# Performance work log

Hardware: AMD Instinct MI355X
Metric: run time of the kernel (lower is better)

## Reference

```python
import jax, jax.numpy as jnp
import numpy as np

B, N, D, E = 4, 4096, 1024, 64
EPS = 1e-9
THRESH = 0.2            # second_threshold_eval
CAP_FACTOR = 2.0        # capacity_factor_eval
MIN_EXPERT_CAPACITY = 4


def setup_inputs() -> dict:
    key = jax.random.key(0)
    k1, k2 = jax.random.split(key)
    x = jax.random.normal(k1, (B, N, D), dtype=jnp.float32)
    w_gating = jax.random.normal(k2, (D, E), dtype=jnp.float32)
    return {"x": x, "w_gating": w_gating}


def _cumsum_exclusive(t, axis):
    # exclusive cumsum along `axis` (equivalent to pad-then-cumsum-then-slice)
    return jnp.cumsum(t, axis=axis) - t


def _gating(x, w_gating):
    b, n, d = x.shape
    e = w_gating.shape[-1]
    dt = x.dtype

    gate_logits = jnp.einsum('bnd,de->bne', x, w_gating)   # [b,n,e]
    raw_gates = jax.nn.softmax(gate_logits, axis=-1)

    index_1 = jnp.argmax(raw_gates, axis=-1)               # [b,n]
    gate_1 = jnp.max(raw_gates, axis=-1)                   # [b,n]
    mask_1 = jax.nn.one_hot(index_1, e, dtype=dt)          # [b,n,e]
    density_1_proxy = raw_gates

    gates_without_top_1 = raw_gates * (1.0 - mask_1)
    index_2 = jnp.argmax(gates_without_top_1, axis=-1)
    gate_2 = jnp.max(gates_without_top_1, axis=-1)
    mask_2 = jax.nn.one_hot(index_2, e, dtype=dt)

    denom = gate_1 + gate_2 + EPS
    gate_1 = gate_1 / denom
    gate_2 = gate_2 / denom

    # load-balancing aux loss
    density_1 = jnp.mean(mask_1, axis=-2)                  # [b,e]
    density_proxy = jnp.mean(density_1_proxy, axis=-2)     # [b,e]
    loss = jnp.mean(density_proxy * density_1) * float(e * e)

    # second-expert policy: 'threshold'
    mask_2 = mask_2 * (gate_2 > THRESH).astype(dt)[..., None]

    expert_capacity = max(min(n, int(n * CAP_FACTOR / e)), MIN_EXPERT_CAPACITY)
    cap_f = float(expert_capacity)

    # capacity routing for top-1
    position_in_expert_1 = _cumsum_exclusive(mask_1, axis=-2) * mask_1
    mask_1 = mask_1 * (position_in_expert_1 < cap_f).astype(dt)
    mask_1_count = jnp.sum(mask_1, axis=-2, keepdims=True)  # [b,1,e]
    mask_1_flat = jnp.sum(mask_1, axis=-1)                  # [b,n]
    position_in_expert_1 = jnp.sum(position_in_expert_1, axis=-1)  # [b,n]
    gate_1 = gate_1 * mask_1_flat

    # capacity routing for top-2 (offset by top-1 counts)
    position_in_expert_2 = (_cumsum_exclusive(mask_2, axis=-2) + mask_1_count) * mask_2
    mask_2 = mask_2 * (position_in_expert_2 < cap_f).astype(dt)
    mask_2_flat = jnp.sum(mask_2, axis=-1)
    position_in_expert_2 = jnp.sum(position_in_expert_2, axis=-1)
    gate_2 = gate_2 * mask_2_flat

    # one_hot with out-of-range index -> all zeros, matching safe_one_hot's clipping
    oh_e1 = jax.nn.one_hot(index_1, e, dtype=dt)
    oh_e2 = jax.nn.one_hot(index_2, e, dtype=dt)
    oh_c1 = jax.nn.one_hot(position_in_expert_1.astype(jnp.int32), expert_capacity, dtype=dt)
    oh_c2 = jax.nn.one_hot(position_in_expert_2.astype(jnp.int32), expert_capacity, dtype=dt)

    combine_tensor = (
        (gate_1 * mask_1_flat)[..., None, None] * oh_e1[..., :, None] * oh_c1[..., None, :]
        + (gate_2 * mask_2_flat)[..., None, None] * oh_e2[..., :, None] * oh_c2[..., None, :]
    )  # [b,n,e,capacity]

    router_z_loss = jnp.mean(jnp.sum(jax.nn.logsumexp(gate_logits, axis=-1), axis=-1))
    return combine_tensor, loss, router_z_loss


def reference(x, w_gating):
    combine_tensor, loss, router_z_loss = _gating(x, w_gating)
    dispatch_tensor = (combine_tensor != 0).astype(combine_tensor.dtype)
    return dispatch_tensor, combine_tensor, loss, router_z_loss
```

## Files before the change

kernel.cpp:

```cpp
#include <hip/hip_runtime.h>


#define B_DIM 4
#define N_DIM 4096
#define D_DIM 1024
#define E_DIM 64
#define CAP   128
#define NTOK  (B_DIM * N_DIM)
#define TM    32
#define TK    64

#define WS_IDX1  0
#define WS_IDX2  65536
#define WS_G1    131072
#define WS_G2    196608
#define WS_POS1  262144
#define WS_POS2  327680
#define WS_CNT1  393216
#define WS_DENS  394240
#define WS_ZSUM  395264

__global__ __launch_bounds__(256) void gating_kernel(
    const float* __restrict__ x, const float* __restrict__ w,
    int* __restrict__ idx1, int* __restrict__ idx2,
    float* __restrict__ g1o, float* __restrict__ g2o,
    int* __restrict__ pos2, float* __restrict__ dens, float* __restrict__ zsum) {
  __shared__ float  As[TM][68];
  __shared__ float  Bs[TK][E_DIM];
  __shared__ double Ld[TM][65];

  const int t = threadIdx.x;
  const int tokBase = blockIdx.x * TM;
  const int e4 = t & 15;
  const int tokg = t >> 4;
  const int tok0 = 2 * tokg, e0 = 4 * e4;

  double acc[2][4] = {};

  for (int k0 = 0; k0 < D_DIM; k0 += TK) {
    {
      const int d4 = t & 15, row = t >> 4;
      float4 va = *(const float4*)(x + (size_t)(tokBase + row) * D_DIM + k0 + 4 * d4);
      float4 vb = *(const float4*)(x + (size_t)(tokBase + row + 16) * D_DIM + k0 + 4 * d4);
      *(float4*)&As[row][4 * d4] = va;
      *(float4*)&As[row + 16][4 * d4] = vb;
    }
    {
      const float4* wsrc = (const float4*)(w + (size_t)k0 * E_DIM);
      float4* bdst = (float4*)&Bs[0][0];
      bdst[t]       = wsrc[t];
      bdst[t + 256] = wsrc[t + 256];
      bdst[t + 512] = wsrc[t + 512];
      bdst[t + 768] = wsrc[t + 768];
    }
    __syncthreads();
#pragma unroll 8
    for (int kk = 0; kk < TK; ++kk) {
      float a0 = As[tok0][kk], a1 = As[tok0 + 1][kk];
      float4 bv = *(float4*)&Bs[kk][e0];
      double da0 = (double)a0, da1 = (double)a1;
      double b0 = (double)bv.x, b1 = (double)bv.y, b2 = (double)bv.z, b3 = (double)bv.w;
      acc[0][0] += da0 * b0; acc[0][1] += da0 * b1; acc[0][2] += da0 * b2; acc[0][3] += da0 * b3;
      acc[1][0] += da1 * b0; acc[1][1] += da1 * b1; acc[1][2] += da1 * b2; acc[1][3] += da1 * b3;
    }
    __syncthreads();
  }

#pragma unroll
  for (int i = 0; i < 2; ++i)
#pragma unroll
    for (int j = 0; j < 4; ++j) Ld[tok0 + i][e0 + j] = acc[i][j];
  __syncthreads();

  const int wave = t >> 6;
  const int lane = t & 63;
  const int b = tokBase >> 12;
  float densacc = 0.f, zacc = 0.f;

  for (int s = 0; s < 8; ++s) {
    const int tok = wave * 8 + s;
    const double l = Ld[tok][lane];

    double mv = l; int mi = lane;
#pragma unroll
    for (int off = 32; off; off >>= 1) {
      double ov = __shfl_xor(mv, off);
      int oi = __shfl_xor(mi, off);
      if (ov > mv || (ov == mv && oi < mi)) { mv = ov; mi = oi; }
    }
    float p = expf((float)(l - mv));
    float sum = p;
#pragma unroll
    for (int off = 32; off; off >>= 1) sum += __shfl_xor(sum, off);

    double l2 = (lane == mi) ? -1.0e300 : l;
    double mv2 = l2; int mi2 = lane;
#pragma unroll
    for (int off = 32; off; off >>= 1) {
      double ov = __shfl_xor(mv2, off);
      int oi = __shfl_xor(mi2, off);
      if (ov > mv2 || (ov == mv2 && oi < mi2)) { mv2 = ov; mi2 = oi; }
    }

    float gate1 = 1.0f / sum;
    float gate2 = expf((float)(mv2 - mv)) / sum;
    float denom = gate1 + gate2 + 1e-9f;
    float g1n = gate1 / denom, g2n = gate2 / denom;
    int i2eff = (g2n > 0.2f) ? mi2 : -1;
    float lse = (float)mv + logf(sum);

    densacc += p;
    if (lane == 0) {
      const int gt = tokBase + tok;
      idx1[gt] = mi; idx2[gt] = i2eff;
      g1o[gt] = g1n; g2o[gt] = g2n;
      pos2[gt] = (1 << 20);
      zacc += lse;
    }
  }
  atomicAdd(&dens[(b << 6) + lane], densacc);
  if (lane == 0) atomicAdd(zsum, zacc);
}

__global__ __launch_bounds__(64) void scan_kernel(
    const int* __restrict__ idx1, const int* __restrict__ idx2,
    int* __restrict__ pos1, int* __restrict__ pos2, int* __restrict__ cnt1) {
  const int bid = blockIdx.x;
  const int b = bid >> 6, e = bid & 63;
  const int lane = threadIdx.x;
  const int base = b * N_DIM;
  const unsigned long long lmask = (1ull << lane) - 1ull;

  int run = 0;
#pragma unroll 4
  for (int ch = 0; ch < N_DIM / 64; ++ch) {
    const int tok = base + ch * 64 + lane;
    const bool m = (idx1[tok] == e);
    unsigned long long bal = __ballot(m);
    if (m) pos1[tok] = run + __popcll(bal & lmask);
    run += __popcll(bal);
  }
  if (lane == 0) cnt1[bid] = run;

  const int off = run < CAP ? run : CAP;
  int run2 = 0;
#pragma unroll 4
  for (int ch = 0; ch < N_DIM / 64; ++ch) {
    const int tok = base + ch * 64 + lane;
    const bool m = (idx2[tok] == e);
    unsigned long long bal = __ballot(m);
    if (m) pos2[tok] = off + run2 + __popcll(bal & lmask);
    run2 += __popcll(bal);
  }
}

__global__ __launch_bounds__(256) void scatter_kernel(
    const int* __restrict__ idx1, const int* __restrict__ idx2,
    const float* __restrict__ g1, const float* __restrict__ g2,
    const int* __restrict__ pos1, const int* __restrict__ pos2,
    const int* __restrict__ cnt1, const float* __restrict__ dens,
    const float* __restrict__ zsum, float* __restrict__ out, size_t half) {
  const int t = blockIdx.x * 256 + threadIdx.x;
  float* dispatch = out;
  float* combine = out + half;

  const int i1 = idx1[t], p1 = pos1[t];
  if (p1 < CAP) {
    const size_t off = ((size_t)t * E_DIM + i1) * CAP + p1;
    combine[off] = g1[t];
    dispatch[off] = 1.0f;
  }
  const int i2 = idx2[t];
  if (i2 >= 0) {
    const int p2 = pos2[t];
    if (p2 < CAP) {
      const size_t off = ((size_t)t * E_DIM + i2) * CAP + p2;
      combine[off] = g2[t];
      dispatch[off] = 1.0f;
    }
  }

  if (blockIdx.x == 0 && threadIdx.x < 64) {
    const int lane = threadIdx.x;
    float partial = 0.f;
#pragma unroll
    for (int k = 0; k < 4; ++k) {
      const int i = lane * 4 + k;
      partial += dens[i] * (float)cnt1[i];
    }
#pragma unroll
    for (int off = 32; off; off >>= 1) partial += __shfl_xor(partial, off);
    if (lane == 0) {
      out[2 * half]     = partial * (1.0f / 1048576.0f);
      out[2 * half + 1] = zsum[0] * 0.25f;
    }
  }
}

extern "C" void kernel_launch(void* const* d_in, const int* in_sizes, int n_in,
                              void* d_out, int out_size, void* d_ws, size_t ws_size,
                              hipStream_t stream) {
  const float* x = (const float*)d_in[0];
  const float* w = (const float*)d_in[1];
  float* out = (float*)d_out;
  char* ws = (char*)d_ws;

  int*   idx1 = (int*)(ws + WS_IDX1);
  int*   idx2 = (int*)(ws + WS_IDX2);
  float* g1   = (float*)(ws + WS_G1);
  float* g2   = (float*)(ws + WS_G2);
  int*   pos1 = (int*)(ws + WS_POS1);
  int*   pos2 = (int*)(ws + WS_POS2);
  int*   cnt1 = (int*)(ws + WS_CNT1);
  float* dens = (float*)(ws + WS_DENS);
  float* zsum = (float*)(ws + WS_ZSUM);

  const size_t half = ((size_t)out_size - 2) / 2;

  hipMemsetAsync(d_out, 0, (size_t)out_size * sizeof(float), stream);
  hipMemsetAsync(ws + WS_DENS, 0, 256 * sizeof(float) + sizeof(float), stream);

  gating_kernel<<<NTOK / TM, 256, 0, stream>>>(x, w, idx1, idx2, g1, g2, pos2, dens, zsum);
  scan_kernel<<<B_DIM * E_DIM, 64, 0, stream>>>(idx1, idx2, pos1, pos2, cnt1);
  scatter_kernel<<<NTOK / 256, 256, 0, stream>>>(idx1, idx2, g1, g2, pos1, pos2,
                                                 cnt1, dens, zsum, out, half);
}
```

Before: 1.181 ms.

## Fuse output zeroing into gating kernel and merge scan with scatter

Replaces the full-output hipMemset with extra blocks in the gating kernel that zero the output using float4 stores, so the zeroing runs alongside the gating GEMM. The scan and scatter kernels are merged into one kernel where four waves each scan a quarter of the tokens, combine their counts through shared memory, and write dispatch and combine entries directly. This removes the pos/cnt workspace round trips and one launch. The aux loss is now accumulated by atomic adds across blocks, and the GEMM shared memory is aliased to cut LDS use.

```diff
diff --git a/kernel.cpp b/kernel.cpp
--- a/kernel.cpp
+++ b/kernel.cpp
@@ -9,27 +9,40 @@
 #define NTOK  (B_DIM * N_DIM)
 #define TM    32
 #define TK    64
+#define GATE_BLOCKS 512
+#define ZERO_BLOCKS 8192
 
 #define WS_IDX1  0
 #define WS_IDX2  65536
 #define WS_G1    131072
 #define WS_G2    196608
-#define WS_POS1  262144
-#define WS_POS2  327680
-#define WS_CNT1  393216
-#define WS_DENS  394240
-#define WS_ZSUM  395264
-
-__global__ __launch_bounds__(256) void gating_kernel(
+#define WS_DENS  262144
+#define WS_ZSUM  263168
+
+__global__ __launch_bounds__(256) void fused_gating_zero(
     const float* __restrict__ x, const float* __restrict__ w,
     int* __restrict__ idx1, int* __restrict__ idx2,
     float* __restrict__ g1o, float* __restrict__ g2o,
-    int* __restrict__ pos2, float* __restrict__ dens, float* __restrict__ zsum) {
-  __shared__ float  As[TM][68];
-  __shared__ float  Bs[TK][E_DIM];
-  __shared__ double Ld[TM][65];
-
+    float* __restrict__ dens, float* __restrict__ zsum,
+    float* __restrict__ out, size_t half) {
+  __shared__ __align__(16) char smem[(TM * 68 + TK * E_DIM) * 4];
   const int t = threadIdx.x;
+
+  if (blockIdx.x >= GATE_BLOCKS) {
+    const int zb = blockIdx.x - GATE_BLOCKS;
+    float4* o4 = (float4*)out;
+    const size_t base = (size_t)zb * (256 * 32) + t;
+    const float4 z = make_float4(0.f, 0.f, 0.f, 0.f);
+#pragma unroll
+    for (int i = 0; i < 32; ++i) o4[base + (size_t)i * 256] = z;
+    if (zb == 0 && t == 0) { out[2 * half] = 0.f; out[2 * half + 1] = 0.f; }
+    return;
+  }
+
+  float (*As)[68]   = (float(*)[68])smem;
+  float (*Bs)[E_DIM] = (float(*)[E_DIM])(smem + TM * 68 * 4);
+  double (*Ld)[65]  = (double(*)[65])smem;
+
   const int tokBase = blockIdx.x * TM;
   const int e4 = t & 15;
   const int tokg = t >> 4;
@@ -114,7 +127,6 @@
       const int gt = tokBase + tok;
       idx1[gt] = mi; idx2[gt] = i2eff;
       g1o[gt] = g1n; g2o[gt] = g2n;
-      pos2[gt] = (1 << 20);
       zacc += lse;
     }
   }
@@ -122,78 +134,88 @@
   if (lane == 0) atomicAdd(zsum, zacc);
 }
 
-__global__ __launch_bounds__(64) void scan_kernel(
+__global__ __launch_bounds__(256) void scan_scatter(
     const int* __restrict__ idx1, const int* __restrict__ idx2,
-    int* __restrict__ pos1, int* __restrict__ pos2, int* __restrict__ cnt1) {
+    const float* __restrict__ g1, const float* __restrict__ g2,
+    const float* __restrict__ dens, const float* __restrict__ zsum,
+    float* __restrict__ out, size_t half) {
   const int bid = blockIdx.x;
   const int b = bid >> 6, e = bid & 63;
-  const int lane = threadIdx.x;
-  const int base = b * N_DIM;
+  const int wv = threadIdx.x >> 6, lane = threadIdx.x & 63;
+  const int tokBase = b * N_DIM + wv * 1024;
   const unsigned long long lmask = (1ull << lane) - 1ull;
-
-  int run = 0;
-#pragma unroll 4
-  for (int ch = 0; ch < N_DIM / 64; ++ch) {
-    const int tok = base + ch * 64 + lane;
-    const bool m = (idx1[tok] == e);
-    unsigned long long bal = __ballot(m);
-    if (m) pos1[tok] = run + __popcll(bal & lmask);
-    run += __popcll(bal);
-  }
-  if (lane == 0) cnt1[bid] = run;
-
-  const int off = run < CAP ? run : CAP;
-  int run2 = 0;
-#pragma unroll 4
-  for (int ch = 0; ch < N_DIM / 64; ++ch) {
-    const int tok = base + ch * 64 + lane;
-    const bool m = (idx2[tok] == e);
-    unsigned long long bal = __ballot(m);
-    if (m) pos2[tok] = off + run2 + __popcll(bal & lmask);
-    run2 += __popcll(bal);
-  }
-}
-
-__global__ __launch_bounds__(256) void scatter_kernel(
-    const int* __restrict__ idx1, const int* __restrict__ idx2,
-    const float* __restrict__ g1, const float* __restrict__ g2,
-    const int* __restrict__ pos1, const int* __restrict__ pos2,
-    const int* __restrict__ cnt1, const float* __restrict__ dens,
-    const float* __restrict__ zsum, float* __restrict__ out, size_t half) {
-  const int t = blockIdx.x * 256 + threadIdx.x;
+  __shared__ int wcnt[4];
+
   float* dispatch = out;
   float* combine = out + half;
-
-  const int i1 = idx1[t], p1 = pos1[t];
-  if (p1 < CAP) {
-    const size_t off = ((size_t)t * E_DIM + i1) * CAP + p1;
-    combine[off] = g1[t];
-    dispatch[off] = 1.0f;
-  }
-  const int i2 = idx2[t];
-  if (i2 >= 0) {
-    const int p2 = pos2[t];
-    if (p2 < CAP) {
-      const size_t off = ((size_t)t * E_DIM + i2) * CAP + p2;
-      combine[off] = g2[t];
-      dispatch[off] = 1.0f;
-    }
-  }
-
-  if (blockIdx.x == 0 && threadIdx.x < 64) {
-    const int lane = threadIdx.x;
-    float partial = 0.f;
-#pragma unroll
-    for (int k = 0; k < 4; ++k) {
-      const int i = lane * 4 + k;
-      partial += dens[i] * (float)cnt1[i];
-    }
-#pragma unroll
-    for (int off = 32; off; off >>= 1) partial += __shfl_xor(partial, off);
-    if (lane == 0) {
-      out[2 * half]     = partial * (1.0f / 1048576.0f);
-      out[2 * half + 1] = zsum[0] * 0.25f;
-    }
+  unsigned long long bal[16];
+
+  int c = 0;
+#pragma unroll
+  for (int ch = 0; ch < 16; ++ch) {
+    bool m = (idx1[tokBase + ch * 64 + lane] == e);
+    bal[ch] = __ballot(m);
+    c += __popcll(bal[ch]);
+  }
+  if (lane == 0) wcnt[wv] = c;
+  __syncthreads();
+  int pre = 0, tot = 0;
+#pragma unroll
+  for (int wvi = 0; wvi < 4; ++wvi) {
+    int v = wcnt[wvi];
+    if (wvi < wv) pre += v;
+    tot += v;
+  }
+  int run = pre;
+#pragma unroll
+  for (int ch = 0; ch < 16; ++ch) {
+    unsigned long long bb = bal[ch];
+    if ((bb >> lane) & 1ull) {
+      int p = run + __popcll(bb & lmask);
+      if (p < CAP) {
+        int tok = tokBase + ch * 64 + lane;
+        size_t off = ((size_t)tok * E_DIM + e) * CAP + p;
+        dispatch[off] = 1.0f;
+        combine[off] = g1[tok];
+      }
+    }
+    run += __popcll(bb);
+  }
+  __syncthreads();
+
+  const int off0 = tot < CAP ? tot : CAP;
+  int c2 = 0;
+#pragma unroll
+  for (int ch = 0; ch < 16; ++ch) {
+    bool m = (idx2[tokBase + ch * 64 + lane] == e);
+    bal[ch] = __ballot(m);
+    c2 += __popcll(bal[ch]);
+  }
+  if (lane == 0) wcnt[wv] = c2;
+  __syncthreads();
+  int pre2 = 0;
+#pragma unroll
+  for (int wvi = 0; wvi < 4; ++wvi)
+    if (wvi < wv) pre2 += wcnt[wvi];
+  int run2 = off0 + pre2;
+#pragma unroll
+  for (int ch = 0; ch < 16; ++ch) {
+    unsigned long long bb = bal[ch];
+    if ((bb >> lane) & 1ull) {
+      int p = run2 + __popcll(bb & lmask);
+      if (p < CAP) {
+        int tok = tokBase + ch * 64 + lane;
+        size_t off = ((size_t)tok * E_DIM + e) * CAP + p;
+        dispatch[off] = 1.0f;
+        combine[off] = g2[tok];
+      }
+    }
+    run2 += __popcll(bb);
+  }
+
+  if (threadIdx.x == 0) {
+    atomicAdd(&out[2 * half], dens[bid] * (float)tot * (1.0f / 1048576.0f));
+    if (bid == 0) out[2 * half + 1] = zsum[0] * 0.25f;
   }
 }
 
@@ -209,19 +231,16 @@
   int*   idx2 = (int*)(ws + WS_IDX2);
   float* g1   = (float*)(ws + WS_G1);
   float* g2   = (float*)(ws + WS_G2);
-  int*   pos1 = (int*)(ws + WS_POS1);
-  int*   pos2 = (int*)(ws + WS_POS2);
-  int*   cnt1 = (int*)(ws + WS_CNT1);
   float* dens = (float*)(ws + WS_DENS);
   float* zsum = (float*)(ws + WS_ZSUM);
 
   const size_t half = ((size_t)out_size - 2) / 2;
 
-  hipMemsetAsync(d_out, 0, (size_t)out_size * sizeof(float), stream);
-  hipMemsetAsync(ws + WS_DENS, 0, 256 * sizeof(float) + sizeof(float), stream);
-
-  gating_kernel<<<NTOK / TM, 256, 0, stream>>>(x, w, idx1, idx2, g1, g2, pos2, dens, zsum);
-  scan_kernel<<<B_DIM * E_DIM, 64, 0, stream>>>(idx1, idx2, pos1, pos2, cnt1);
-  scatter_kernel<<<NTOK / 256, 256, 0, stream>>>(idx1, idx2, g1, g2, pos1, pos2,
-                                                 cnt1, dens, zsum, out, half);
+  hipMemsetAsync(ws + WS_DENS, 0, 257 * sizeof(float), stream);
+
+  fused_gating_zero<<<GATE_BLOCKS + ZERO_BLOCKS, 256, 0, stream>>>(
+      x, w, idx1, idx2, g1, g2, dens, zsum, out, half);
+
+  scan_scatter<<<B_DIM * E_DIM, 256, 0, stream>>>(idx1, idx2, g1, g2,
+                                                  dens, zsum, out, half);
 }
```

Result: faster. 1.111 ms (-5.9%).
